# Performance work log

Measured on AMD Instinct MI355X. Metric: run time of the kernel, lower is better.

## Reference

```python
import jax, jax.numpy as jnp
import numpy as np

N = 100000      # nodes
E = 1600000     # edges (avg degree 16)
D_IN = 128
D_OUT = 128
ORDER = 2
EPS = 1e-9


def setup_inputs() -> dict:
    key = jax.random.key(0)
    ks = jax.random.split(key, 8)
    inp = {}
    inp["vecs"] = jax.random.normal(ks[0], (N, D_IN), dtype=jnp.float32)
    inp["adj_vals"] = jax.random.uniform(ks[1], (E,), dtype=jnp.float32)
    inp["row"] = jax.random.randint(ks[2], (E,), 0, N)
    inp["col"] = jax.random.randint(ks[3], (E,), 0, N)
    lim = float(np.sqrt(6.0 / (D_IN + D_OUT)))  # glorot uniform
    for o in range(ORDER + 1):
        inp[f"W{o}"] = jax.random.uniform(ks[4 + o], (D_IN, D_OUT), dtype=jnp.float32, minval=-lim, maxval=lim)
        inp[f"b{o}"] = jnp.zeros((D_OUT,), jnp.float32)
        inp[f"off{o}"] = jnp.zeros((1, D_OUT), jnp.float32)
        inp[f"sc{o}"] = jnp.ones((1, D_OUT), jnp.float32)
    return inp


def _spmm(vals, row, col, x):
    # sparse_tensor_dense_matmul: out[r] = sum_e vals[e] * x[col[e]] for row[e]==r
    return jax.ops.segment_sum(vals[:, None] * x[col], row, num_segments=N)


def _f_nonlinear(v, W, b, off, sc):
    vw = jax.nn.relu(v @ W + b)
    mean = jnp.mean(vw, axis=1, keepdims=True)
    var = jnp.var(vw, axis=1, keepdims=True)
    # tf.nn.batch_normalization with per-row moments, eps=1e-9
    return sc * (vw - mean) * jax.lax.rsqrt(var + EPS) + off


def reference(vecs, adj_vals, row, col,
              W0, W1, W2, b0, b1, b2,
              off0, off1, off2, sc0, sc1, sc2):
    Ws = [W0, W1, W2]
    bs = [b0, b1, b2]
    offs = [off0, off1, off2]
    scs = [sc0, sc1, sc2]
    # vecs_hop[k] = A^k @ vecs (dropout=0 -> identity)
    hops = [vecs]
    for _ in range(ORDER):
        hops.append(_spmm(adj_vals, row, col, hops[-1]))
    outs = [_f_nonlinear(hops[o], Ws[o], bs[o], offs[o], scs[o]) for o in range(ORDER + 1)]
    ret = outs[0]
    for o in range(1, ORDER + 1):  # aggr == 'mean' (actually a sum in the source)
        ret = ret + outs[o]
    return ret
```

## Files before the change

### kernel.cpp

```cpp
#include <hip/hip_runtime.h>
#include <math.h>

#define NN 100000
#define DD 128
#define NB 391
#define RP_PAD 100004

typedef short bf16x8 __attribute__((ext_vector_type(8)));
typedef float f32x4  __attribute__((ext_vector_type(4)));
typedef unsigned uint4v __attribute__((ext_vector_type(4)));

__device__ __forceinline__ unsigned f2bf_rne(float f) {
    unsigned u = __float_as_uint(f);
    return (u + 0x7FFFu + ((u >> 16) & 1u)) >> 16;
}
__device__ __forceinline__ unsigned packbf(float a, float b) {
    return f2bf_rne(a) | (f2bf_rne(b) << 16);
}
__device__ __forceinline__ float bf_lo(unsigned u) { return __uint_as_float(u << 16); }
__device__ __forceinline__ float bf_hi(unsigned u) { return __uint_as_float(u & 0xFFFF0000u); }

__device__ __forceinline__ int2 ldnt_edge(const int2* p) {
    long long v = __builtin_nontemporal_load((const long long*)p);
    int2 r;
    r.x = (int)(v & 0xffffffffll);
    r.y = (int)(((unsigned long long)v) >> 32);
    return r;
}

__global__ __launch_bounds__(256) void convert_all(
    const float* __restrict__ vecs, unsigned short* __restrict__ vecs_bf,
    const float* __restrict__ W0, const float* __restrict__ W1,
    const float* __restrict__ W2, unsigned short* __restrict__ Wt,
    int* __restrict__ bcnt, int n8)
{
    const int b = blockIdx.x;
    const int t = threadIdx.x;
    if (b < 24) {
        const float* W = (b < 8) ? W0 : ((b < 16) ? W1 : W2);
        unsigned short* dst = Wt + (b >> 3) * DD * DD;
        int idx = (b & 7) * 256 + t;
        int n = idx >> 4;
        int kc = (idx & 15) * 8;
        unsigned r[4];
        #pragma unroll
        for (int j = 0; j < 4; j++) {
            float a = W[(kc + 2 * j) * DD + n];
            float c = W[(kc + 2 * j + 1) * DD + n];
            r[j] = packbf(a, c);
        }
        *(uint4*)(dst + n * DD + kc) = make_uint4(r[0], r[1], r[2], r[3]);
    } else if (b == 24) {
        for (int j = t; j < 512; j += 256) bcnt[j] = 0;
    } else {
        int i = (b - 25) * 256 + t;
        if (i >= n8) return;
        f32x4 a = __builtin_nontemporal_load((const f32x4*)vecs + (size_t)i * 2);
        f32x4 c = __builtin_nontemporal_load((const f32x4*)vecs + (size_t)i * 2 + 1);
        uint4v o;
        o.x = packbf(a.x, a.y); o.y = packbf(a.z, a.w);
        o.z = packbf(c.x, c.y); o.w = packbf(c.z, c.w);
        ((uint4v*)vecs_bf)[i] = o;
    }
}

__global__ __launch_bounds__(256) void bucket_scatter(
    const int* __restrict__ row, const int* __restrict__ col,
    const float* __restrict__ vals, int* __restrict__ bcnt,
    int2* __restrict__ ep_raw, int E, int CAP)
{
    __shared__ int cnt[NB];
    __shared__ int base[NB];
    for (int j = threadIdx.x; j < NB; j += 256) cnt[j] = 0;
    __syncthreads();
    int cb = blockIdx.x * 8192;
    int ce = min(cb + 8192, E);
    for (int j = cb + threadIdx.x; j < ce; j += 256)
        atomicAdd(&cnt[row[j] >> 8], 1);
    __syncthreads();
    for (int j = threadIdx.x; j < NB; j += 256) {
        int c = cnt[j];
        base[j] = c ? (j * CAP + atomicAdd(&bcnt[j], c)) : 0;
        cnt[j] = 0;
    }
    __syncthreads();
    for (int j = cb + threadIdx.x; j < ce; j += 256) {
        int r = row[j];
        int c = __builtin_nontemporal_load(col + j);
        float v = __builtin_nontemporal_load(vals + j);
        int b = r >> 8;
        int off = atomicAdd(&cnt[b], 1);
        unsigned meta = (unsigned)c | ((unsigned)(r & 255) << 17);
        ep_raw[base[b] + off] = make_int2((int)meta, __float_as_int(v));
    }
}

__global__ __launch_bounds__(512) void bucket_scan(
    const int* __restrict__ bcnt, int* __restrict__ bbase)
{
    __shared__ int sh[512];
    int t = threadIdx.x;
    int v = (t < NB) ? bcnt[t] : 0;
    sh[t] = v;
    __syncthreads();
    for (int off = 1; off < 512; off <<= 1) {
        int u = (t >= off) ? sh[t - off] : 0;
        __syncthreads();
        sh[t] += u;
        __syncthreads();
    }
    if (t < NB) bbase[t] = sh[t] - v;
    if (t == NB - 1) bbase[NB] = sh[NB - 1];
}

__global__ __launch_bounds__(256) void bucket_to_csr(
    const int* __restrict__ bbase, const int2* __restrict__ ep_raw,
    int* __restrict__ row_ptr, int2* __restrict__ ep, int CAP, int N, int E)
{
    __shared__ int rcnt[256];
    __shared__ int rcur[256];
    __shared__ int wsum[4];
    const int b = blockIdx.x;
    const int t = threadIdx.x;
    const int dst = bbase[b];
    const int cnt = bbase[b + 1] - dst;
    const int src = b * CAP;

    rcnt[t] = 0;
    __syncthreads();
    for (int j = t; j < cnt; j += 256)
        atomicAdd(&rcnt[(unsigned)ep_raw[src + j].x >> 17], 1);
    __syncthreads();

    int v = rcnt[t];
    int lane = t & 63;
    int inc = v;
    #pragma unroll
    for (int off = 1; off < 64; off <<= 1) {
        int u = __shfl_up(inc, off, 64);
        if (lane >= off) inc += u;
    }
    if (lane == 63) wsum[t >> 6] = inc;
    __syncthreads();
    int woff = 0;
    for (int i = 0; i < (t >> 6); i++) woff += wsum[i];
    int excl = woff + inc - v;

    int grow = b * 256 + t;
    if (grow < N) row_ptr[grow] = dst + excl;
    rcur[t] = excl;
    __syncthreads();

    for (int j = t; j < cnt; j += 256) {
        int2 rec = ldnt_edge(ep_raw + src + j);
        unsigned meta = (unsigned)rec.x;
        int rlo = meta >> 17;
        int c = (int)(meta & 0x1FFFFu);
        int p = atomicAdd(&rcur[rlo], 1);
        ep[dst + p] = make_int2(c, rec.y);
    }
    if (b == 0 && t == 0) row_ptr[N] = E;
}

__device__ __forceinline__ void accum8(float* acc, uint4 u, float v) {
    acc[0] += v * bf_lo(u.x); acc[1] += v * bf_hi(u.x);
    acc[2] += v * bf_lo(u.y); acc[3] += v * bf_hi(u.y);
    acc[4] += v * bf_lo(u.z); acc[5] += v * bf_hi(u.z);
    acc[6] += v * bf_lo(u.w); acc[7] += v * bf_hi(u.w);
}

__global__ __launch_bounds__(256) void spmm_bf16(
    const uint4* __restrict__ x, const int* __restrict__ row_ptr,
    const int2* __restrict__ ep, uint4* __restrict__ out, int N)
{
    int t = blockIdx.x * 256 + threadIdx.x;
    int g = t >> 4;
    int lane = t & 15;
    if (g >= N) return;

    int s = row_ptr[g];
    int e = row_ptr[g + 1];
    float acc[8] = {0.f, 0.f, 0.f, 0.f, 0.f, 0.f, 0.f, 0.f};

    int k = s;
    for (; k + 8 <= e; k += 8) {
        int2 E0 = ep[k + 0], E1 = ep[k + 1], E2 = ep[k + 2], E3 = ep[k + 3];
        int2 E4 = ep[k + 4], E5 = ep[k + 5], E6 = ep[k + 6], E7 = ep[k + 7];
        uint4 X0 = x[(size_t)E0.x * 16 + lane];
        uint4 X1 = x[(size_t)E1.x * 16 + lane];
        uint4 X2 = x[(size_t)E2.x * 16 + lane];
        uint4 X3 = x[(size_t)E3.x * 16 + lane];
        uint4 X4 = x[(size_t)E4.x * 16 + lane];
        uint4 X5 = x[(size_t)E5.x * 16 + lane];
        uint4 X6 = x[(size_t)E6.x * 16 + lane];
        uint4 X7 = x[(size_t)E7.x * 16 + lane];
        accum8(acc, X0, __int_as_float(E0.y));
        accum8(acc, X1, __int_as_float(E1.y));
        accum8(acc, X2, __int_as_float(E2.y));
        accum8(acc, X3, __int_as_float(E3.y));
        accum8(acc, X4, __int_as_float(E4.y));
        accum8(acc, X5, __int_as_float(E5.y));
        accum8(acc, X6, __int_as_float(E6.y));
        accum8(acc, X7, __int_as_float(E7.y));
    }
    for (; k + 4 <= e; k += 4) {
        int2 E0 = ep[k + 0], E1 = ep[k + 1], E2 = ep[k + 2], E3 = ep[k + 3];
        uint4 X0 = x[(size_t)E0.x * 16 + lane];
        uint4 X1 = x[(size_t)E1.x * 16 + lane];
        uint4 X2 = x[(size_t)E2.x * 16 + lane];
        uint4 X3 = x[(size_t)E3.x * 16 + lane];
        accum8(acc, X0, __int_as_float(E0.y));
        accum8(acc, X1, __int_as_float(E1.y));
        accum8(acc, X2, __int_as_float(E2.y));
        accum8(acc, X3, __int_as_float(E3.y));
    }
    for (; k < e; k++) {
        int2 E0 = ep[k];
        uint4 X0 = x[(size_t)E0.x * 16 + lane];
        accum8(acc, X0, __int_as_float(E0.y));
    }

    uint4 o;
    o.x = packbf(acc[0], acc[1]); o.y = packbf(acc[2], acc[3]);
    o.z = packbf(acc[4], acc[5]); o.w = packbf(acc[6], acc[7]);
    out[(size_t)g * 16 + lane] = o;
}

__device__ __forceinline__ void bn_accum(
    f32x4* acc, const float* __restrict__ bias, const float* __restrict__ off,
    const float* __restrict__ sc, int i, float facc[8][4])
{
    float bc[8], sv[8], ov[8];
    #pragma unroll
    for (int ct = 0; ct < 8; ct++) {
        int c = ct * 16 + i;
        bc[ct] = bias[c]; sv[ct] = sc[c]; ov[ct] = off[c];
    }
    float s[4] = {0.f, 0.f, 0.f, 0.f};
    float qq[4] = {0.f, 0.f, 0.f, 0.f};
    #pragma unroll
    for (int ct = 0; ct < 8; ct++) {
        #pragma unroll
        for (int r = 0; r < 4; r++) {
            float v = fmaxf(acc[ct][r] + bc[ct], 0.f);
            acc[ct][r] = v;
            s[r] += v;
            qq[r] += v * v;
        }
    }
    #pragma unroll
    for (int r = 0; r < 4; r++) {
        #pragma unroll
        for (int m = 1; m <= 8; m <<= 1) {
            s[r]  += __shfl_xor(s[r],  m, 64);
            qq[r] += __shfl_xor(qq[r], m, 64);
        }
    }
    #pragma unroll
    for (int r = 0; r < 4; r++) {
        float mn = s[r] * 0.0078125f;
        float var = qq[r] * 0.0078125f - mn * mn;
        float rs = rsqrtf(var + 1e-9f);
        #pragma unroll
        for (int ct = 0; ct < 8; ct++)
            facc[ct][r] += sv[ct] * (acc[ct][r] - mn) * rs + ov[ct];
    }
}

__global__ __launch_bounds__(256) void fused_dense_mfma(
    const unsigned short* __restrict__ h0,
    const unsigned short* __restrict__ h1,
    const unsigned short* __restrict__ h2,
    const unsigned short* __restrict__ Wt,
    const float* __restrict__ b0, const float* __restrict__ b1,
    const float* __restrict__ b2,
    const float* __restrict__ off0, const float* __restrict__ off1,
    const float* __restrict__ off2,
    const float* __restrict__ sc0, const float* __restrict__ sc1,
    const float* __restrict__ sc2,
    float* __restrict__ out, int N)
{
    __shared__ uint4 Bl[2048];

    const int tid  = threadIdx.x;
    const int wave = tid >> 6;
    const int lane = tid & 63;
    const int i    = lane & 15;
    const int q    = lane >> 4;
    const int slab = blockIdx.x * 64 + wave * 16;

    int arow = slab + i;
    if (arow >= N) arow = N - 1;

    const unsigned short* hops[3] = {h0, h1, h2};
    const float* bs[3]  = {b0, b1, b2};
    const float* ofs[3] = {off0, off1, off2};
    const float* scs[3] = {sc0, sc1, sc2};
    const bf16x8* Bv = (const bf16x8*)Bl;

    float facc[8][4];
    #pragma unroll
    for (int ct = 0; ct < 8; ct++)
        #pragma unroll
        for (int r = 0; r < 4; r++) facc[ct][r] = 0.f;

    for (int o = 0; o < 3; o++) {
        const uint4* Wg = (const uint4*)(Wt + o * DD * DD);
        #pragma unroll
        for (int j = 0; j < 8; j++) {
            int c  = j * 256 + tid;
            int nn = c & 127;
            int kc = c >> 7;
            Bl[kc * 128 + nn] = Wg[nn * 16 + kc];
        }
        __syncthreads();

        const unsigned short* arow_p = hops[o] + (size_t)arow * DD + q * 8;
        f32x4 acc[8];
        #pragma unroll
        for (int ct = 0; ct < 8; ct++) acc[ct] = (f32x4){0.f, 0.f, 0.f, 0.f};
        #pragma unroll
        for (int kb = 0; kb < 4; kb++) {
            bf16x8 a = __builtin_nontemporal_load((const bf16x8*)(arow_p + kb * 32));
            const int kc = kb * 4 + q;
            #pragma unroll
            for (int ct = 0; ct < 8; ct++) {
                bf16x8 b = Bv[kc * 128 + ct * 16 + i];
                acc[ct] = __builtin_amdgcn_mfma_f32_16x16x32_bf16(a, b, acc[ct], 0, 0, 0);
            }
        }
        bn_accum(acc, bs[o], ofs[o], scs[o], i, facc);
        __syncthreads();
    }

    #pragma unroll
    for (int r = 0; r < 4; r++) {
        int orow = slab + q * 4 + r;
        if (orow < N) {
            float* op = out + (size_t)orow * DD + i;
            #pragma unroll
            for (int ct = 0; ct < 8; ct++)
                __builtin_nontemporal_store(facc[ct][r], op + ct * 16);
        }
    }
}

extern "C" void kernel_launch(void* const* d_in, const int* in_sizes, int n_in,
                              void* d_out, int out_size, void* d_ws, size_t ws_size,
                              hipStream_t stream)
{
    const float* vecs = (const float*)d_in[0];
    const float* adj  = (const float*)d_in[1];
    const int*   row  = (const int*)d_in[2];
    const int*   col  = (const int*)d_in[3];
    const float* W0   = (const float*)d_in[4];
    const float* b0   = (const float*)d_in[5];
    const float* off0 = (const float*)d_in[6];
    const float* sc0  = (const float*)d_in[7];
    const float* W1   = (const float*)d_in[8];
    const float* b1   = (const float*)d_in[9];
    const float* off1 = (const float*)d_in[10];
    const float* sc1  = (const float*)d_in[11];
    const float* W2   = (const float*)d_in[12];
    const float* b2   = (const float*)d_in[13];
    const float* off2 = (const float*)d_in[14];
    const float* sc2  = (const float*)d_in[15];

    const int E = in_sizes[1];
    const int N = NN;

    const int avg = (E + NB - 1) / NB;
    const int CAP = (avg + 8 * (int)sqrt((double)avg) + 79) & ~15;

    unsigned short* hop1_bf = (unsigned short*)d_ws;
    unsigned short* hop2_bf = hop1_bf + (size_t)N * DD;
    unsigned short* vecs_bf = hop2_bf + (size_t)N * DD;
    unsigned short* Wt_bf   = vecs_bf + (size_t)N * DD;
    int*   row_ptr  = (int*)(Wt_bf + 3 * DD * DD);
    int*   bcnt     = row_ptr + RP_PAD;
    int*   bbase    = bcnt + 512;
    int2*  ep_raw   = (int2*)(bbase + 512);
    int2*  epack    = ep_raw + (size_t)NB * CAP;

    const int n8 = N * DD / 8;
    convert_all<<<25 + (n8 + 255) / 256, 256, 0, stream>>>(
        vecs, vecs_bf, W0, W1, W2, Wt_bf, bcnt, n8);

    const int cb = (E + 8191) / 8192;
    bucket_scatter<<<cb, 256, 0, stream>>>(row, col, adj, bcnt, ep_raw, E, CAP);
    bucket_scan<<<1, 512, 0, stream>>>(bcnt, bbase);
    bucket_to_csr<<<NB, 256, 0, stream>>>(bbase, ep_raw, row_ptr, epack, CAP, N, E);

    int sb = (N * 16 + 255) / 256;
    spmm_bf16<<<sb, 256, 0, stream>>>(
        (const uint4*)vecs_bf, row_ptr, epack, (uint4*)hop1_bf, N);
    spmm_bf16<<<sb, 256, 0, stream>>>(
        (const uint4*)hop1_bf, row_ptr, epack, (uint4*)hop2_bf, N);

    const int db = (N + 63) / 64;
    fused_dense_mfma<<<db, 256, 0, stream>>>(
        vecs_bf, hop1_bf, hop2_bf, Wt_bf,
        b0, b1, b2, off0, off1, off2, sc0, sc1, sc2,
        (float*)d_out, N);
}
```

Before: 359.8 us.

## Fold bucket scan and input conversion into CSR finish kernel

Removes the single-block bucket_scan kernel by having each CSR-building block compute its own prefix offset through a shared-memory reduction over the preceding bucket counts. The vecs/W bf16 conversion blocks are merged into the same launch, and the counter zeroing becomes a hipMemsetAsync. This cuts two launches and a serial single-block step, at the cost of redundant per-block prefix reductions and a memset call.

```diff
diff --git a/kernel.cpp b/kernel.cpp
--- a/kernel.cpp
+++ b/kernel.cpp
@@ -26,42 +26,6 @@
     r.x = (int)(v & 0xffffffffll);
     r.y = (int)(((unsigned long long)v) >> 32);
     return r;
-}
-
-__global__ __launch_bounds__(256) void convert_all(
-    const float* __restrict__ vecs, unsigned short* __restrict__ vecs_bf,
-    const float* __restrict__ W0, const float* __restrict__ W1,
-    const float* __restrict__ W2, unsigned short* __restrict__ Wt,
-    int* __restrict__ bcnt, int n8)
-{
-    const int b = blockIdx.x;
-    const int t = threadIdx.x;
-    if (b < 24) {
-        const float* W = (b < 8) ? W0 : ((b < 16) ? W1 : W2);
-        unsigned short* dst = Wt + (b >> 3) * DD * DD;
-        int idx = (b & 7) * 256 + t;
-        int n = idx >> 4;
-        int kc = (idx & 15) * 8;
-        unsigned r[4];
-        #pragma unroll
-        for (int j = 0; j < 4; j++) {
-            float a = W[(kc + 2 * j) * DD + n];
-            float c = W[(kc + 2 * j + 1) * DD + n];
-            r[j] = packbf(a, c);
-        }
-        *(uint4*)(dst + n * DD + kc) = make_uint4(r[0], r[1], r[2], r[3]);
-    } else if (b == 24) {
-        for (int j = t; j < 512; j += 256) bcnt[j] = 0;
-    } else {
-        int i = (b - 25) * 256 + t;
-        if (i >= n8) return;
-        f32x4 a = __builtin_nontemporal_load((const f32x4*)vecs + (size_t)i * 2);
-        f32x4 c = __builtin_nontemporal_load((const f32x4*)vecs + (size_t)i * 2 + 1);
-        uint4v o;
-        o.x = packbf(a.x, a.y); o.y = packbf(a.z, a.w);
-        o.z = packbf(c.x, c.y); o.w = packbf(c.z, c.w);
-        ((uint4v*)vecs_bf)[i] = o;
-    }
 }
 
 __global__ __launch_bounds__(256) void bucket_scatter(
@@ -95,35 +59,62 @@
     }
 }
 
-__global__ __launch_bounds__(512) void bucket_scan(
-    const int* __restrict__ bcnt, int* __restrict__ bbase)
-{
-    __shared__ int sh[512];
-    int t = threadIdx.x;
-    int v = (t < NB) ? bcnt[t] : 0;
-    sh[t] = v;
-    __syncthreads();
-    for (int off = 1; off < 512; off <<= 1) {
-        int u = (t >= off) ? sh[t - off] : 0;
-        __syncthreads();
-        sh[t] += u;
-        __syncthreads();
-    }
-    if (t < NB) bbase[t] = sh[t] - v;
-    if (t == NB - 1) bbase[NB] = sh[NB - 1];
-}
-
-__global__ __launch_bounds__(256) void bucket_to_csr(
-    const int* __restrict__ bbase, const int2* __restrict__ ep_raw,
-    int* __restrict__ row_ptr, int2* __restrict__ ep, int CAP, int N, int E)
-{
+__global__ __launch_bounds__(256) void csr_finish_convert(
+    const int* __restrict__ bcnt, const int2* __restrict__ ep_raw,
+    int* __restrict__ row_ptr, int2* __restrict__ ep,
+    const float* __restrict__ vecs, unsigned short* __restrict__ vecs_bf,
+    const float* __restrict__ W0, const float* __restrict__ W1,
+    const float* __restrict__ W2, unsigned short* __restrict__ Wt,
+    int CAP, int N, int E, int n8)
+{
+    const int b = blockIdx.x;
+    const int t = threadIdx.x;
+
+    if (b >= NB) {
+        if (b < NB + 24) {
+            const int b2 = b - NB;
+            const float* W = (b2 < 8) ? W0 : ((b2 < 16) ? W1 : W2);
+            unsigned short* dst = Wt + (b2 >> 3) * DD * DD;
+            int idx = (b2 & 7) * 256 + t;
+            int n = idx >> 4;
+            int kc = (idx & 15) * 8;
+            unsigned r[4];
+            #pragma unroll
+            for (int j = 0; j < 4; j++) {
+                float a = W[(kc + 2 * j) * DD + n];
+                float c = W[(kc + 2 * j + 1) * DD + n];
+                r[j] = packbf(a, c);
+            }
+            *(uint4*)(dst + n * DD + kc) = make_uint4(r[0], r[1], r[2], r[3]);
+        } else {
+            int i = (b - NB - 24) * 256 + t;
+            if (i >= n8) return;
+            f32x4 a = __builtin_nontemporal_load((const f32x4*)vecs + (size_t)i * 2);
+            f32x4 c = __builtin_nontemporal_load((const f32x4*)vecs + (size_t)i * 2 + 1);
+            uint4v o;
+            o.x = packbf(a.x, a.y); o.y = packbf(a.z, a.w);
+            o.z = packbf(c.x, c.y); o.w = packbf(c.z, c.w);
+            ((uint4v*)vecs_bf)[i] = o;
+        }
+        return;
+    }
+
+    __shared__ int red[256];
     __shared__ int rcnt[256];
     __shared__ int rcur[256];
     __shared__ int wsum[4];
-    const int b = blockIdx.x;
-    const int t = threadIdx.x;
-    const int dst = bbase[b];
-    const int cnt = bbase[b + 1] - dst;
+
+    int part = 0;
+    for (int j = t; j < b; j += 256) part += bcnt[j];
+    red[t] = part;
+    __syncthreads();
+    #pragma unroll
+    for (int off = 128; off > 0; off >>= 1) {
+        if (t < off) red[t] += red[t + off];
+        __syncthreads();
+    }
+    const int dst = red[0];
+    const int cnt = bcnt[b];
     const int src = b * CAP;
 
     rcnt[t] = 0;
@@ -378,18 +369,20 @@
     unsigned short* Wt_bf   = vecs_bf + (size_t)N * DD;
     int*   row_ptr  = (int*)(Wt_bf + 3 * DD * DD);
     int*   bcnt     = row_ptr + RP_PAD;
-    int*   bbase    = bcnt + 512;
-    int2*  ep_raw   = (int2*)(bbase + 512);
+    int2*  ep_raw   = (int2*)(bcnt + 512);
     int2*  epack    = ep_raw + (size_t)NB * CAP;
 
-    const int n8 = N * DD / 8;
-    convert_all<<<25 + (n8 + 255) / 256, 256, 0, stream>>>(
-        vecs, vecs_bf, W0, W1, W2, Wt_bf, bcnt, n8);
+    hipMemsetAsync(bcnt, 0, NB * sizeof(int), stream);
 
     const int cb = (E + 8191) / 8192;
     bucket_scatter<<<cb, 256, 0, stream>>>(row, col, adj, bcnt, ep_raw, E, CAP);
-    bucket_scan<<<1, 512, 0, stream>>>(bcnt, bbase);
-    bucket_to_csr<<<NB, 256, 0, stream>>>(bbase, ep_raw, row_ptr, epack, CAP, N, E);
+
+    const int n8 = N * DD / 8;
+    const int vb = (n8 + 255) / 256;
+    csr_finish_convert<<<NB + 24 + vb, 256, 0, stream>>>(
+        bcnt, ep_raw, row_ptr, epack,
+        vecs, vecs_bf, W0, W1, W2, Wt_bf,
+        CAP, N, E, n8);
 
     int sb = (N * 16 + 255) / 256;
     spmm_bf16<<<sb, 256, 0, stream>>>(
```

Measured after the change: 356.0 us. Within noise of the previous version (-1.0%).
